# Kernel optimization log

Hardware: AMD Instinct MI355X
Metric: run time of the kernel (lower is better)

The kernel has to match this reference:

```python
import jax, jax.numpy as jnp
import numpy as np

L, B, D = 2048, 16, 1024
SCALE_X = (1.0 + 2.0 * float(np.exp(0.0))) ** 0.5  # rescale=True, highway_bias=0 -> sqrt(3)


def setup_inputs() -> dict:
    key = jax.random.key(0)
    k1, k2, k3 = jax.random.split(key, 3)
    x = jax.random.normal(k1, (L, B, D), dtype=jnp.float32)
    c0 = jnp.zeros((B, D), dtype=jnp.float32)
    # Xavier-ish scale (3/d)^0.5 as in reset_parameters
    val_range = (3.0 / D) ** 0.5
    weight = jax.random.uniform(k2, (D, 3 * D), dtype=jnp.float32,
                                minval=-val_range, maxval=val_range)
    weight_c = jax.random.uniform(k3, (2 * D,), dtype=jnp.float32,
                                  minval=-val_range, maxval=val_range)
    bias = jnp.zeros((2 * D,), dtype=jnp.float32)
    return {"x": x, "c0": c0, "weight": weight, "weight_c": weight_c, "bias": bias}


def _sru_forward(x, c0, weight, weight_c, bias):
    # u = x @ W, viewed as [L, B, D, 3] (k = 3)
    u = jnp.einsum('lbi,io->lbo', x, weight).reshape(L, B, D, 3)
    fw, rw = weight_c[:D], weight_c[D:]      # per-feature recurrent gate weights
    fb, rb = bias[:D], bias[D:]              # forget / reset biases
    u0 = u[..., 0]                           # [L, B, D] candidate
    u1 = u[..., 1] + fb                      # forget pre-activation
    u2 = u[..., 2] + rb                      # reset pre-activation
    xp = x * SCALE_X                         # highway term (k==3, skip via x)

    def step(c_prev, inputs):
        u0_t, u1_t, u2_t, xp_t = inputs
        f = jax.nn.sigmoid(u1_t + c_prev * fw)
        r = jax.nn.sigmoid(u2_t + c_prev * rw)
        c = u0_t + (c_prev - u0_t) * f
        g = c  # activation_type == 0 (identity)
        h = xp_t + (g - xp_t) * r
        return c, h

    c_final, h = jax.lax.scan(step, c0, (u0, u1, u2, xp))
    return h, c_final


def reference(x, c0, weight, weight_c, bias):
    return _sru_forward(x, c0, weight, weight_c, bias)
```

## Files before the change

### kernel.cpp

```cpp
#include <hip/hip_runtime.h>
#include <stdint.h>

#define L_DIM 2048
#define B_DIM 16
#define D_DIM 1024
#define M_DIM 32768
#define K_DIM 1024
#define N_DIM 3072
#define SCALE_X 1.7320508075688772f

typedef __attribute__((ext_vector_type(8))) short short8;
typedef __attribute__((ext_vector_type(8))) unsigned short ushort8;
typedef __attribute__((ext_vector_type(4))) float f32x4;

__device__ __forceinline__ float bf2f(uint32_t b) {
    union { uint32_t u; float f; } v; v.u = b << 16; return v.f;
}
__device__ __forceinline__ uint16_t f2bf(float f) {
    union { float f; uint32_t u; } v; v.f = f;
    uint32_t u = v.u;
    return (uint16_t)((u + 0x7FFFu + ((u >> 16) & 1u)) >> 16);
}

__device__ __forceinline__ void gload_lds16(const void* g, void* l) {
    __builtin_amdgcn_global_load_lds(
        (const __attribute__((address_space(1))) void*)g,
        (__attribute__((address_space(3))) void*)l,
        16 , 0, 0);
}

__global__ void prep_w_kernel(const float* __restrict__ w, uint16_t* __restrict__ wt) {
    int i = blockIdx.x * 256 + threadIdx.x;
    int k = i / N_DIM;
    int n = i - k * N_DIM;
    wt[n * K_DIM + k] = f2bf(w[i]);
}

__global__ void __launch_bounds__(256)
prep_x_kernel(const float* __restrict__ x, uint16_t* __restrict__ xb) {
    size_t i = (size_t)blockIdx.x * 256 + threadIdx.x;
    const float4 a = *(const float4*)(x + i * 8);
    const float4 b = *(const float4*)(x + i * 8 + 4);
    ushort8 o;
    o[0] = f2bf(a.x); o[1] = f2bf(a.y); o[2] = f2bf(a.z); o[3] = f2bf(a.w);
    o[4] = f2bf(b.x); o[5] = f2bf(b.y); o[6] = f2bf(b.z); o[7] = f2bf(b.w);
    *(ushort8*)(xb + i * 8) = o;
}

__global__ void __launch_bounds__(256)
gemm_lds_kernel(const uint16_t* __restrict__ Ab,
                const uint16_t* __restrict__ Bt,
                uint16_t* __restrict__ u01,
                uint16_t* __restrict__ u2p)
{
    __shared__ uint16_t As[128 * 32];
    __shared__ uint16_t Bs[128 * 32];

    int bid = blockIdx.x;
    int mg = bid / 192;
    int tt = bid - mg * 192;
    int ntile = tt >> 3;
    int mtile = mg * 8 + (tt & 7);
    int m0 = mtile * 128;
    int n0 = ntile * 128;

    int t = threadIdx.x;
    int lane = t & 63;
    int w = t >> 6;
    int wm = (w >> 1) * 64;
    int wn = (w & 1) * 64;

    f32x4 acc[4][4] = {};

    int frow = lane & 15;
    int fk = (lane >> 4) * 8;

    for (int kt = 0; kt < K_DIM; kt += 32) {
#pragma unroll
        for (int c = 0; c < 2; c++) {
            int idx = c * 256 + t;
            int row = idx >> 2;
            int ko = (idx & 3) * 8;
            gload_lds16(Ab + (size_t)(m0 + row) * K_DIM + kt + ko, As + idx * 8);
        }
#pragma unroll
        for (int c = 0; c < 2; c++) {
            int idx = c * 256 + t;
            int row = idx >> 2;
            int ko = (idx & 3) * 8;
            gload_lds16(Bt + (size_t)(n0 + row) * K_DIM + kt + ko, Bs + idx * 8);
        }
        __syncthreads();

        short8 af[4], bfr[4];
#pragma unroll
        for (int i = 0; i < 4; i++) {
            af[i]  = *(const short8*)(As + (wm + i * 16 + frow) * 32 + fk);
            bfr[i] = *(const short8*)(Bs + (wn + i * 16 + frow) * 32 + fk);
        }
#pragma unroll
        for (int i = 0; i < 4; i++)
#pragma unroll
            for (int j = 0; j < 4; j++)
                acc[i][j] = __builtin_amdgcn_mfma_f32_16x16x32_bf16(af[i], bfr[j], acc[i][j], 0, 0, 0);
        __syncthreads();
    }

    int colf = lane & 15;
    int rowq = (lane >> 4) * 4;
#pragma unroll
    for (int i = 0; i < 4; i++) {
#pragma unroll
        for (int j = 0; j < 4; j++) {
            int gcol = n0 + wn + j * 16 + colf;
            int dq = gcol / 3;
            int cm = gcol - dq * 3;
#pragma unroll
            for (int r = 0; r < 4; r++) {
                int grow = m0 + wm + i * 16 + rowq + r;
                uint16_t v = f2bf(acc[i][j][r]);
                if (cm < 2) u01[(size_t)grow * 2048 + dq * 2 + cm] = v;
                else        u2p[(size_t)grow * 1024 + dq] = v;
            }
        }
    }
}

__global__ void __launch_bounds__(256)
gemm_kernel(const float* __restrict__ A32,
            const uint16_t* __restrict__ Bt,
            uint16_t* __restrict__ u01,
            uint16_t* __restrict__ u2p)
{
    __shared__ uint16_t As[128 * 32];
    __shared__ uint16_t Bs[128 * 32];

    int bid = blockIdx.x;
    int mg = bid / 192;
    int tt = bid - mg * 192;
    int ntile = tt >> 3;
    int mtile = mg * 8 + (tt & 7);
    int m0 = mtile * 128;
    int n0 = ntile * 128;

    int t = threadIdx.x;
    int lane = t & 63;
    int w = t >> 6;
    int wm = (w >> 1) * 64;
    int wn = (w & 1) * 64;

    f32x4 acc[4][4] = {};

    int frow = lane & 15;
    int fk = (lane >> 4) * 8;

    for (int kt = 0; kt < K_DIM; kt += 32) {
#pragma unroll
        for (int c = 0; c < 4; c++) {
            int idx = c * 256 + t;
            int row = idx >> 3;
            int ko = (idx & 7) * 4;
            float4 v = *(const float4*)(A32 + (size_t)(m0 + row) * K_DIM + kt + ko);
            ushort4 o;
            o.x = f2bf(v.x); o.y = f2bf(v.y); o.z = f2bf(v.z); o.w = f2bf(v.w);
            *(ushort4*)(As + row * 32 + ko) = o;
        }
#pragma unroll
        for (int c = 0; c < 2; c++) {
            int idx = c * 256 + t;
            int row = idx >> 2;
            int ko = (idx & 3) * 8;
            short8 v = *(const short8*)(Bt + (size_t)(n0 + row) * K_DIM + kt + ko);
            *(short8*)(Bs + row * 32 + ko) = v;
        }
        __syncthreads();

        short8 af[4], bfr[4];
#pragma unroll
        for (int i = 0; i < 4; i++) {
            af[i]  = *(const short8*)(As + (wm + i * 16 + frow) * 32 + fk);
            bfr[i] = *(const short8*)(Bs + (wn + i * 16 + frow) * 32 + fk);
        }
#pragma unroll
        for (int i = 0; i < 4; i++)
#pragma unroll
            for (int j = 0; j < 4; j++)
                acc[i][j] = __builtin_amdgcn_mfma_f32_16x16x32_bf16(af[i], bfr[j], acc[i][j], 0, 0, 0);
        __syncthreads();
    }

    int colf = lane & 15;
    int rowq = (lane >> 4) * 4;
#pragma unroll
    for (int i = 0; i < 4; i++) {
#pragma unroll
        for (int j = 0; j < 4; j++) {
            int gcol = n0 + wn + j * 16 + colf;
            int dq = gcol / 3;
            int cm = gcol - dq * 3;
#pragma unroll
            for (int r = 0; r < 4; r++) {
                int grow = m0 + wm + i * 16 + rowq + r;
                uint16_t v = f2bf(acc[i][j][r]);
                if (cm < 2) u01[(size_t)grow * 2048 + dq * 2 + cm] = v;
                else        u2p[(size_t)grow * 1024 + dq] = v;
            }
        }
    }
}

__global__ void __launch_bounds__(64)
scan_kernel(const uint32_t* u01,
            const uint16_t* __restrict__ u2p,
            const float* __restrict__ x,
            const float* __restrict__ c0,
            const float* __restrict__ wc,
            const float* __restrict__ bias,
            float* out)
{
    int cid = blockIdx.x * 64 + threadIdx.x;
    int d = cid & (D_DIM - 1);
    float fw = wc[d], rw = wc[D_DIM + d];
    float fb = bias[d], rb = bias[D_DIM + d];
    float c = c0[cid];

    constexpr int P = 16;
    const int STEP = B_DIM * D_DIM;
    uint32_t b01[P];
    uint16_t b2v[P];
    float bx[P];
#pragma unroll
    for (int j = 0; j < P; j++) {
        b01[j] = u01[cid + j * STEP];
        b2v[j] = u2p[cid + j * STEP];
        bx[j]  = x[cid + j * STEP];
    }

    for (int lb = 0; lb < L_DIM; lb += P) {
#pragma unroll
        for (int j = 0; j < P; j++) {
            int l = lb + j;
            uint32_t v01 = b01[j];
            float u2 = bf2f((uint32_t)b2v[j]);
            float xp = bx[j] * SCALE_X;

            int ln = l + P; if (ln > L_DIM - 1) ln = L_DIM - 1;
            int ri = cid + ln * STEP;
            b01[j] = u01[ri];
            b2v[j] = u2p[ri];
            bx[j]  = x[ri];

            float u0 = bf2f(v01 & 0xFFFFu);
            float u1 = bf2f(v01 >> 16);

            float ef = __expf(-(u1 + fb + c * fw));
            float er = __expf(-(u2 + rb + c * rw));
            float f = __builtin_amdgcn_rcpf(1.0f + ef);
            float r = __builtin_amdgcn_rcpf(1.0f + er);
            c = u0 + (c - u0) * f;
            float h = xp + (c - xp) * r;
            out[l * STEP + cid] = h;
        }
    }
    out[L_DIM * STEP + cid] = c;
}

extern "C" void kernel_launch(void* const* d_in, const int* in_sizes, int n_in,
                              void* d_out, int out_size, void* d_ws, size_t ws_size,
                              hipStream_t stream) {
    const float* x    = (const float*)d_in[0];
    const float* c0   = (const float*)d_in[1];
    const float* w    = (const float*)d_in[2];
    const float* wc   = (const float*)d_in[3];
    const float* bias = (const float*)d_in[4];

    uint16_t* wt  = (uint16_t*)d_ws;
    uint16_t* u2p = (uint16_t*)((char*)d_ws + 6291456);
    const size_t XB_OFF = 6291456 + (size_t)M_DIM * D_DIM * 2;
    const size_t WS_NEED = XB_OFF + (size_t)M_DIM * K_DIM * 2;

    uint16_t* u01 = (uint16_t*)d_out;
    float* out = (float*)d_out;

    prep_w_kernel<<<(K_DIM * N_DIM) / 256, 256, 0, stream>>>(w, wt);

    if (ws_size >= WS_NEED) {
        uint16_t* xb = (uint16_t*)((char*)d_ws + XB_OFF);
        prep_x_kernel<<<(M_DIM * K_DIM / 8) / 256, 256, 0, stream>>>(x, xb);
        gemm_lds_kernel<<<(M_DIM / 128) * (N_DIM / 128), 256, 0, stream>>>(xb, wt, u01, u2p);
    } else {
        gemm_kernel<<<(M_DIM / 128) * (N_DIM / 128), 256, 0, stream>>>(x, wt, u01, u2p);
    }

    scan_kernel<<<(B_DIM * D_DIM) / 64, 64, 0, stream>>>((const uint32_t*)u01, u2p, x,
                                                         c0, wc, bias, out);
}
```

Baseline: 731.0 us.

## Replace bf16 GEMM with 256x256 double-buffered, swizzled, phase-interleaved MFMA kernel

Replaces the 128x128 single-buffer LDS GEMM with a 512-thread 256x256 tile kernel that uses a K-step of 64, double-buffered LDS (128KB), XOR-swizzled LDS layout and async global-to-LDS loads. The loads for the next K tile are interleaved with four quadrant MFMA phases, and setprio is raised around the MFMA bursts. The aim is to hide global load latency, cut the number of barriers and avoid LDS bank conflicts so the kernel becomes more compute-bound. In exchange it needs far more LDS and registers, which limits occupancy, and it depends on hand-tuned waitcnt ordering.

```diff
diff --git a/kernel.cpp b/kernel.cpp
--- a/kernel.cpp
+++ b/kernel.cpp
@@ -22,11 +22,21 @@
     return (uint16_t)((u + 0x7FFFu + ((u >> 16) & 1u)) >> 16);
 }
 
-__device__ __forceinline__ void gload_lds16(const void* g, void* l) {
+__device__ __forceinline__ void gl16(const uint16_t* g, uint16_t* l) {
     __builtin_amdgcn_global_load_lds(
         (const __attribute__((address_space(1))) void*)g,
         (__attribute__((address_space(3))) void*)l,
         16 , 0, 0);
+}
+
+__device__ __forceinline__ void fence_all() {
+    asm volatile("" ::: "memory");
+    __builtin_amdgcn_sched_barrier(0);
+}
+__device__ __forceinline__ void barrier_hard() {
+    fence_all();
+    __builtin_amdgcn_s_barrier();
+    fence_all();
 }
 
 __global__ void prep_w_kernel(const float* __restrict__ w, uint16_t* __restrict__ wt) {
@@ -47,69 +57,127 @@
     *(ushort8*)(xb + i * 8) = o;
 }
 
-__global__ void __launch_bounds__(256)
-gemm_lds_kernel(const uint16_t* __restrict__ Ab,
+__global__ void __launch_bounds__(512, 2)
+gemm_8ph_kernel(const uint16_t* __restrict__ Ab,
                 const uint16_t* __restrict__ Bt,
                 uint16_t* __restrict__ u01,
                 uint16_t* __restrict__ u2p)
 {
-    __shared__ uint16_t As[128 * 32];
-    __shared__ uint16_t Bs[128 * 32];
+    __shared__ uint16_t lds[65536];
 
     int bid = blockIdx.x;
-    int mg = bid / 192;
-    int tt = bid - mg * 192;
+    int mg = bid / 96;
+    int tt = bid - mg * 96;
     int ntile = tt >> 3;
     int mtile = mg * 8 + (tt & 7);
-    int m0 = mtile * 128;
-    int n0 = ntile * 128;
+    int m0 = mtile * 256;
+    int n0 = ntile * 256;
 
     int t = threadIdx.x;
     int lane = t & 63;
     int w = t >> 6;
-    int wm = (w >> 1) * 64;
-    int wn = (w & 1) * 64;
-
-    f32x4 acc[4][4] = {};
+    int wm = (w >> 2) * 128;
+    int wn = (w & 3) * 64;
+
+    int row0 = t >> 3;
+    int slot = t & 7;
+    int swz_c = (slot ^ (row0 & 7)) * 8;
+    const uint16_t* pA = Ab + (((size_t)(m0 + row0)) << 10) + swz_c;
+    const uint16_t* pB = Bt + (((size_t)(n0 + row0)) << 10) + swz_c;
 
     int frow = lane & 15;
-    int fk = (lane >> 4) * 8;
-
-    for (int kt = 0; kt < K_DIM; kt += 32) {
-#pragma unroll
-        for (int c = 0; c < 2; c++) {
-            int idx = c * 256 + t;
-            int row = idx >> 2;
-            int ko = (idx & 3) * 8;
-            gload_lds16(Ab + (size_t)(m0 + row) * K_DIM + kt + ko, As + idx * 8);
-        }
-#pragma unroll
-        for (int c = 0; c < 2; c++) {
-            int idx = c * 256 + t;
-            int row = idx >> 2;
-            int ko = (idx & 3) * 8;
-            gload_lds16(Bt + (size_t)(n0 + row) * K_DIM + kt + ko, Bs + idx * 8);
-        }
-        __syncthreads();
-
-        short8 af[4], bfr[4];
-#pragma unroll
-        for (int i = 0; i < 4; i++) {
-            af[i]  = *(const short8*)(As + (wm + i * 16 + frow) * 32 + fk);
-            bfr[i] = *(const short8*)(Bs + (wn + i * 16 + frow) * 32 + fk);
-        }
-#pragma unroll
-        for (int i = 0; i < 4; i++)
-#pragma unroll
-            for (int j = 0; j < 4; j++)
-                acc[i][j] = __builtin_amdgcn_mfma_f32_16x16x32_bf16(af[i], bfr[j], acc[i][j], 0, 0, 0);
-        __syncthreads();
-    }
+    int fkb = (lane >> 4) * 16;
+
+    f32x4 acc[8][4] = {};
+    short8 aF[4][2];
+    short8 bF[4][2];
+
+#define STAGE(hh, Tn) { \
+    const uint16_t* gs = (((hh) < 2) ? pA : pB) + ((size_t)((hh) & 1) * 131072) + (size_t)(Tn) * 64; \
+    uint16_t* ld = lds + nxtO + (hh) * 8192 + t * 8; \
+    gl16(gs, ld); gl16(gs + 65536, ld + 4096); }
+
+#define RD_A(mh) { \
+    _Pragma("unroll") for (int mf = 0; mf < 4; mf++) \
+    _Pragma("unroll") for (int ks = 0; ks < 2; ks++) { \
+        int r = wm + (mh) * 64 + mf * 16 + frow; \
+        int cb = (ks * 64 + fkb) ^ ((r & 7) << 4); \
+        aF[mf][ks] = *(const short8*)(lds + curA + r * 64 + (cb >> 1)); } }
+
+#define RD_B() { \
+    _Pragma("unroll") for (int nf = 0; nf < 4; nf++) \
+    _Pragma("unroll") for (int ks = 0; ks < 2; ks++) { \
+        int r = wn + nf * 16 + frow; \
+        int cb = (ks * 64 + fkb) ^ ((r & 7) << 4); \
+        bF[nf][ks] = *(const short8*)(lds + curB + r * 64 + (cb >> 1)); } }
+
+#define QM(mh, nh) { \
+    __builtin_amdgcn_s_setprio(1); \
+    _Pragma("unroll") for (int mf = 0; mf < 4; mf++) \
+    _Pragma("unroll") for (int nj = 0; nj < 2; nj++) \
+    _Pragma("unroll") for (int ks = 0; ks < 2; ks++) \
+        acc[(mh) * 4 + mf][(nh) * 2 + nj] = __builtin_amdgcn_mfma_f32_16x16x32_bf16( \
+            aF[mf][ks], bF[(nh) * 2 + nj][ks], acc[(mh) * 4 + mf][(nh) * 2 + nj], 0, 0, 0); \
+    __builtin_amdgcn_s_setprio(0); }
+
+    {
+        int nxtO = 0;
+        STAGE(0, 0); STAGE(1, 0); STAGE(2, 0); STAGE(3, 0);
+    }
+
+    for (int T = 0; T < 15; ++T) {
+        int cur = T & 1;
+        int curA = cur * 32768;
+        int curB = curA + 16384;
+        int nxtO = (cur ^ 1) * 32768;
+
+        barrier_hard();
+        STAGE(0, T + 1);
+        fence_all();
+        asm volatile("s_waitcnt vmcnt(2)" ::: "memory");
+        barrier_hard();
+        RD_B();
+        RD_A(0);
+        QM(0, 0);
+        fence_all();
+        STAGE(1, T + 1);
+        fence_all();
+        QM(0, 1);
+        RD_A(1);
+        fence_all();
+        STAGE(2, T + 1);
+        fence_all();
+        QM(1, 1);
+        fence_all();
+        STAGE(3, T + 1);
+        fence_all();
+        QM(1, 0);
+    }
+
+    {
+        int curA = 32768;
+        int curB = curA + 16384;
+        barrier_hard();
+        asm volatile("s_waitcnt vmcnt(0)" ::: "memory");
+        barrier_hard();
+        RD_B();
+        RD_A(0);
+        QM(0, 0);
+        QM(0, 1);
+        RD_A(1);
+        QM(1, 1);
+        QM(1, 0);
+    }
+
+#undef STAGE
+#undef RD_A
+#undef RD_B
+#undef QM
 
     int colf = lane & 15;
     int rowq = (lane >> 4) * 4;
 #pragma unroll
-    for (int i = 0; i < 4; i++) {
+    for (int i = 0; i < 8; i++) {
 #pragma unroll
         for (int j = 0; j < 4; j++) {
             int gcol = n0 + wn + j * 16 + colf;
@@ -287,7 +355,7 @@
     if (ws_size >= WS_NEED) {
         uint16_t* xb = (uint16_t*)((char*)d_ws + XB_OFF);
         prep_x_kernel<<<(M_DIM * K_DIM / 8) / 256, 256, 0, stream>>>(x, xb);
-        gemm_lds_kernel<<<(M_DIM / 128) * (N_DIM / 128), 256, 0, stream>>>(xb, wt, u01, u2p);
+        gemm_8ph_kernel<<<(M_DIM / 256) * (N_DIM / 256), 512, 0, stream>>>(xb, wt, u01, u2p);
     } else {
         gemm_kernel<<<(M_DIM / 128) * (N_DIM / 128), 256, 0, stream>>>(x, wt, u01, u2p);
     }
```

After: 690.6 us. 1.06x faster.
